# Kernel tuning notes

Measured on AMD Instinct MI355X. Metric: run time of the kernel, lower is better.

The kernel has to match this reference:

```python
import math
import jax, jax.numpy as jnp
import numpy as np

B, N, T, H = 4, 64, 384, 256
LAGS = (1, 5, 21)
L = len(LAGS)
NU = 500  # peer-universe size for rank buffers
TOPK = 8
LN_EPS = 1e-5


def setup_inputs() -> dict:
    key = jax.random.key(0)
    ks = jax.random.split(key, 24)
    s = 1.0 / np.sqrt(H)

    def lin(i):
        w = jax.random.uniform(ks[i], (H, H), jnp.float32, -s, s)
        b = jax.random.uniform(ks[i + 1], (H,), jnp.float32, -s, s)
        return w, b

    wq_w, wq_b = lin(0)
    wk_w, wk_b = lin(2)
    wv_w, wv_b = lin(4)
    f1_w, f1_b = lin(6)
    f2_w, f2_b = lin(8)
    return dict(
        target_h=jax.random.normal(ks[10], (B, T, H), jnp.float32),
        peer_h=jax.random.normal(ks[11], (B, N, T, H), jnp.float32),
        wq_w=wq_w, wq_b=wq_b, wk_w=wk_w, wk_b=wk_b, wv_w=wv_w, wv_b=wv_b,
        f1_w=f1_w, f1_b=f1_b, f2_w=f2_w, f2_b=f2_b,
        ln_g=jnp.ones((H,), jnp.float32),
        ln_b=jnp.zeros((H,), jnp.float32),
        alpha=jnp.float32(0.1),
        log_rank_strength=jnp.log(jnp.clip(jax.random.uniform(ks[12], (L, NU, NU)), 1e-6, None)),
        peer_mask=jnp.ones((B, N), dtype=bool),
        rank_topk_mask=jax.random.uniform(ks[13], (L, NU, NU)) < 0.2,
        target_id=jax.random.randint(ks[14], (B,), 0, NU),
        peer_id=jax.random.randint(ks[15], (B, N), 0, NU),
    )


def _forward(target_h, peer_h, wq_w, wq_b, wk_w, wk_b, wv_w, wv_b,
             f1_w, f1_b, f2_w, f2_b, ln_g, ln_b, alpha, log_rank_strength,
             peer_mask, rank_topk_mask, target_id, peer_id):
    lags = jnp.array(LAGS, dtype=jnp.int32)
    t_idx = jnp.arange(T, dtype=jnp.int32)[None, :] - lags[:, None]   # [L,T]
    valid_time = t_idx >= 0                                           # [L,T]
    t_idx_c = jnp.maximum(t_idx, 0)

    # lag-gathered peer features: [B,N,L,T,H] -> [B,T,N,L,H]
    peer_h_lag = jnp.transpose(peer_h[:, :, t_idx_c, :], (0, 3, 1, 2, 4))

    Q = target_h @ wq_w.T + wq_b                  # [B,T,H]
    K = peer_h_lag @ wk_w.T + wk_b                # [B,T,N,L,H]
    # delta-valued V path (use_delta_value=True): current minus lagged
    peer_h_now = jnp.transpose(peer_h, (0, 2, 1, 3))[:, :, :, None, :]  # [B,T,N,1,H]
    V = (peer_h_now - peer_h_lag) @ wv_w.T + wv_b  # [B,T,N,L,H]

    logits = jnp.einsum('bth,btnlh->btnl', Q, K) / math.sqrt(H)  # [B,T,N,L]

    # Bennett soft bias (use_bennett=True)
    tgt_b = jnp.broadcast_to(target_id[:, None], (B, N))          # [B,N]
    prior = jnp.transpose(log_rank_strength[:, peer_id, tgt_b], (1, 2, 0))  # [B,N,L]
    logits = logits + alpha * prior[:, None, :, :]

    neg_inf = jnp.float32(-jnp.inf)
    logits = jnp.where(valid_time.T[None, :, None, :], logits, neg_inf)      # time validity
    logits = jnp.where(peer_mask[:, None, :, None], logits, neg_inf)         # peer mask
    rmask = jnp.transpose(rank_topk_mask[:, peer_id, tgt_b], (1, 2, 0))      # [B,N,L]
    logits = jnp.where(rmask[:, None, :, :], logits, neg_inf)                # hard rank mask

    NL = N * L
    k = min(TOPK, NL)
    logits_flat = logits.reshape(B, T, NL)
    topk_vals, topk_idx = jax.lax.top_k(logits_flat, k)            # [B,T,k]
    is_inf = jnp.isinf(topk_vals)
    all_inf = jnp.all(is_inf, axis=-1, keepdims=True)
    topk_safe = jnp.where(is_inf, jnp.float32(-1e9), topk_vals)
    weights = jax.nn.softmax(topk_safe, axis=-1)
    weights = weights * (~all_inf).astype(weights.dtype)

    V_flat = V.reshape(B, T, NL, H)
    V_sel = jnp.take_along_axis(V_flat, topk_idx[..., None], axis=2)  # [B,T,k,H]
    ll_y = jnp.sum(weights[..., None] * V_sel, axis=2)                # [B,T,H]

    ffn = jax.nn.elu(ll_y @ f1_w.T + f1_b) @ f2_w.T + f2_b
    x = ll_y + ffn
    mu = jnp.mean(x, axis=-1, keepdims=True)
    var = jnp.var(x, axis=-1, keepdims=True)
    return (x - mu) / jnp.sqrt(var + LN_EPS) * ln_g + ln_b


def reference(target_h, peer_h, wq_w, wq_b, wk_w, wk_b, wv_w, wv_b,
              f1_w, f1_b, f2_w, f2_b, ln_g, ln_b, alpha, log_rank_strength,
              peer_mask, rank_topk_mask, target_id, peer_id):
    return _forward(target_h, peer_h, wq_w, wq_b, wk_w, wk_b, wv_w, wv_b,
                    f1_w, f1_b, f2_w, f2_b, ln_g, ln_b, alpha, log_rank_strength,
                    peer_mask, rank_topk_mask, target_id, peer_id)
```

## Files before the change

### kernel.cpp

```cpp
#include <hip/hip_runtime.h>
#include <hip/hip_bf16.h>


#define NU_ 500

__device__ __forceinline__ bool mask_at(const void* p, long i, int mode){
  if (mode == 1) return ((const unsigned char*)p)[i] != 0;
  if (mode == 2) return ((const unsigned short*)p)[i] != 0;
  return ((const unsigned int*)p)[i] != 0;
}

__global__ void prep_kernel(const float* __restrict__ lrs,
                            const void* __restrict__ pmask, const void* __restrict__ rmask,
                            const int* __restrict__ target_id, const int* __restrict__ peer_id,
                            const float* __restrict__ alpha_p,
                            float* __restrict__ prior)
{
  const int b = blockIdx.x;
  const int c = threadIdx.x;
  if (c >= 192) return;
  const unsigned char* pmB = (const unsigned char*)pmask;
  const unsigned char p0 = pmB[0], p1 = pmB[1];
  int mmode;
  if (p0 == 0x01u)      mmode = (p1 == 0x01u) ? 1 : 0;
  else if (p0 == 0x80u) mmode = 2;
  else                  mmode = 0;

  const int n = c / 3, l = c - n * 3;
  const int pid = peer_id[b * 64 + n];
  const int tgt = target_id[b];
  const long ridx = (long)l * (NU_*NU_) + (long)pid * NU_ + tgt;
  const bool ok = mask_at(pmask, b * 64 + n, mmode) && mask_at(rmask, ridx, mmode);
  prior[b * 192 + c] = ok ? alpha_p[0] * lrs[ridx] : -__builtin_inff();
}

__global__ __launch_bounds__(256) void qproj_kernel(
    const float* __restrict__ xg, const float* __restrict__ wq, const float* __restrict__ wqb,
    const float* __restrict__ wk, const float* __restrict__ wkb,
    float* __restrict__ Qt, float* __restrict__ qb)
{
  __shared__ __align__(16) float xs[8][256];
  __shared__ __align__(16) float qs[8][256];
  const int j = threadIdx.x;
  const int row0 = blockIdx.x * 8;
  #pragma unroll
  for (int r = 0; r < 8; ++r) xs[r][j] = xg[(long)(row0 + r) * 256 + j];
  __syncthreads();

  float acc[8];
  #pragma unroll
  for (int r = 0; r < 8; ++r) acc[r] = 0.f;
  const float4* wrow = (const float4*)(wq + (long)j * 256);
  for (int h8 = 0; h8 < 32; ++h8){
    float4 wa = wrow[h8 * 2], wb = wrow[h8 * 2 + 1];
    const int h = h8 * 8;
    #pragma unroll
    for (int r = 0; r < 8; ++r){
      const float* xr = &xs[r][h];
      acc[r] += xr[0]*wa.x + xr[1]*wa.y + xr[2]*wa.z + xr[3]*wa.w
              + xr[4]*wb.x + xr[5]*wb.y + xr[6]*wb.z + xr[7]*wb.w;
    }
  }
  const float bq = wqb[j];
  #pragma unroll
  for (int r = 0; r < 8; ++r) qs[r][j] = acc[r] + bq;
  __syncthreads();

  float at[8];
  #pragma unroll
  for (int r = 0; r < 8; ++r) at[r] = 0.f;
  for (int h = 0; h < 256; ++h){
    const float w = wk[(long)h * 256 + j];
    #pragma unroll
    for (int r = 0; r < 8; ++r) at[r] += qs[r][h] * w;
  }
  #pragma unroll
  for (int r = 0; r < 8; ++r) Qt[(long)(row0 + r) * 256 + j] = at[r];

  const float bk = wkb[j];
  #pragma unroll
  for (int r = 0; r < 8; ++r) xs[r][j] = qs[r][j] * bk;
  __syncthreads();
  if (j < 8){
    float s = 0.f;
    for (int h = 0; h < 256; ++h) s += xs[j][h];
    qb[row0 + j] = s;
  }
}

__global__ __launch_bounds__(256) void attn_kernel(
    const float* __restrict__ peer_h, const float* __restrict__ Qt,
    const float* __restrict__ qbv, const float* __restrict__ prior,
    float* __restrict__ dvec, float* __restrict__ ssum)
{
  __shared__ __align__(16) float qt_s[256];
  __shared__ float lg[192];
  __shared__ int   seli[8];
  __shared__ float selw[8];
  __shared__ int   allinf_sh;
  const int bt = blockIdx.x;
  const int b = bt / 384, t = bt % 384;
  const int tid = threadIdx.x;
  const float NEG_INF = -__builtin_inff();

  qt_s[tid] = Qt[(long)bt * 256 + tid];
  __syncthreads();
  const float qb = qbv[bt];
  const int lags[3] = {1, 5, 21};

  const int group = tid >> 4, q = tid & 15;
  float qv[16];
  #pragma unroll
  for (int i = 0; i < 4; ++i){
    float4 f = *(const float4*)&qt_s[q * 16 + i * 4];
    qv[i*4] = f.x; qv[i*4+1] = f.y; qv[i*4+2] = f.z; qv[i*4+3] = f.w;
  }

  #pragma unroll
  for (int it = 0; it < 12; ++it){
    const int c = it * 16 + group;
    const int n = c / 3, l = c - n * 3;
    const int lag = lags[l];
    const float pe = prior[b * 192 + c];
    const bool ok = (t >= lag) && (pe > -3.0e38f);
    float logit = NEG_INF;
    if (ok){
      const float4* rp = (const float4*)(peer_h + (((long)(b*64 + n)) * 384 + (t - lag)) * 256);
      float4 u0 = rp[q*4], u1 = rp[q*4+1], u2 = rp[q*4+2], u3 = rp[q*4+3];
      float p = u0.x*qv[0] + u0.y*qv[1] + u0.z*qv[2] + u0.w*qv[3]
              + u1.x*qv[4] + u1.y*qv[5] + u1.z*qv[6] + u1.w*qv[7]
              + u2.x*qv[8] + u2.y*qv[9] + u2.z*qv[10]+ u2.w*qv[11]
              + u3.x*qv[12]+ u3.y*qv[13]+ u3.z*qv[14]+ u3.w*qv[15];
      #pragma unroll
      for (int off = 1; off < 16; off <<= 1) p += __shfl_xor(p, off);
      logit = (p + qb) * 0.0625f + pe;
    }
    if (q == 0) lg[c] = logit;
  }
  __syncthreads();

  if (tid < 64){
    const int lane = tid;
    float v0 = lg[lane], v1 = lg[lane + 64], v2 = lg[lane + 128];
    float sv[8]; int si[8];
    for (int k = 0; k < 8; ++k){
      float mv = v0; int mi = lane;
      if (v1 > mv){ mv = v1; mi = lane + 64; }
      if (v2 > mv){ mv = v2; mi = lane + 128; }
      #pragma unroll
      for (int off = 32; off; off >>= 1){
        float ov = __shfl_xor(mv, off);
        int   oi = __shfl_xor(mi, off);
        if (ov > mv || (ov == mv && oi < mi)){ mv = ov; mi = oi; }
      }
      sv[k] = mv; si[k] = mi;
      if      (mi == lane)       v0 = NEG_INF;
      else if (mi == lane + 64)  v1 = NEG_INF;
      else if (mi == lane + 128) v2 = NEG_INF;
    }
    const int allinf = (sv[0] == NEG_INF) ? 1 : 0;
    const float m = allinf ? -1e9f : sv[0];
    float e[8]; float tot = 0.f;
    #pragma unroll
    for (int k = 0; k < 8; ++k){
      const float s = (sv[k] == NEG_INF) ? -1e9f : sv[k];
      e[k] = expf(s - m);
      tot += e[k];
    }
    if (lane == 0){
      allinf_sh = allinf;
      const float inv = 1.f / tot;
      for (int k = 0; k < 8; ++k){
        seli[k] = si[k];
        selw[k] = allinf ? 0.f : e[k] * inv;
      }
    }
  }
  __syncthreads();

  float acc = 0.f;
  const int h = tid;
  #pragma unroll
  for (int k = 0; k < 8; ++k){
    const float w = selw[k];
    if (w != 0.f){
      const int c = seli[k];
      const int n = c / 3, l = c - n * 3;
      const int tc = t - lags[l];
      const long base = ((long)(b*64 + n)) * 384;
      acc += w * (peer_h[(base + t ) * 256 + h]
                - peer_h[(base + tc) * 256 + h]);
    }
  }
  dvec[(long)bt * 256 + h] = acc;
  if (tid == 0) ssum[bt] = allinf_sh ? 0.f : 1.f;
}

__global__ __launch_bounds__(256) void ffn_kernel(
    const float* __restrict__ dv, const float* __restrict__ sv,
    const float* __restrict__ wv, const float* __restrict__ wvb,
    const float* __restrict__ f1, const float* __restrict__ f1b,
    const float* __restrict__ f2, const float* __restrict__ f2b,
    const float* __restrict__ lng, const float* __restrict__ lnb,
    float* __restrict__ out)
{
  __shared__ __align__(16) float ds[8][256];
  __shared__ __align__(16) float ys[8][256];
  __shared__ float mu_s[8], rs_s[8];
  const int j = threadIdx.x;
  const int row0 = blockIdx.x * 8;
  #pragma unroll
  for (int r = 0; r < 8; ++r) ds[r][j] = dv[(long)(row0 + r) * 256 + j];
  __syncthreads();

  float ll[8];
  {
    #pragma unroll
    for (int r = 0; r < 8; ++r) ll[r] = 0.f;
    const float4* wrow = (const float4*)(wv + (long)j * 256);
    for (int h8 = 0; h8 < 32; ++h8){
      float4 wa = wrow[h8 * 2], wb = wrow[h8 * 2 + 1];
      const int h = h8 * 8;
      #pragma unroll
      for (int r = 0; r < 8; ++r){
        const float* xr = &ds[r][h];
        ll[r] += xr[0]*wa.x + xr[1]*wa.y + xr[2]*wa.z + xr[3]*wa.w
               + xr[4]*wb.x + xr[5]*wb.y + xr[6]*wb.z + xr[7]*wb.w;
      }
    }
    const float bv = wvb[j];
    #pragma unroll
    for (int r = 0; r < 8; ++r) ll[r] += sv[row0 + r] * bv;
  }
  #pragma unroll
  for (int r = 0; r < 8; ++r) ys[r][j] = ll[r];
  __syncthreads();

  {
    float a[8];
    #pragma unroll
    for (int r = 0; r < 8; ++r) a[r] = 0.f;
    const float4* wrow = (const float4*)(f1 + (long)j * 256);
    for (int h8 = 0; h8 < 32; ++h8){
      float4 wa = wrow[h8 * 2], wb = wrow[h8 * 2 + 1];
      const int h = h8 * 8;
      #pragma unroll
      for (int r = 0; r < 8; ++r){
        const float* xr = &ys[r][h];
        a[r] += xr[0]*wa.x + xr[1]*wa.y + xr[2]*wa.z + xr[3]*wa.w
              + xr[4]*wb.x + xr[5]*wb.y + xr[6]*wb.z + xr[7]*wb.w;
      }
    }
    const float b1 = f1b[j];
    #pragma unroll
    for (int r = 0; r < 8; ++r){
      const float x = a[r] + b1;
      ds[r][j] = (x > 0.f) ? x : expm1f(x);
    }
  }
  __syncthreads();

  float xv[8];
  {
    float a[8];
    #pragma unroll
    for (int r = 0; r < 8; ++r) a[r] = 0.f;
    const float4* wrow = (const float4*)(f2 + (long)j * 256);
    for (int h8 = 0; h8 < 32; ++h8){
      float4 wa = wrow[h8 * 2], wb = wrow[h8 * 2 + 1];
      const int h = h8 * 8;
      #pragma unroll
      for (int r = 0; r < 8; ++r){
        const float* xr = &ds[r][h];
        a[r] += xr[0]*wa.x + xr[1]*wa.y + xr[2]*wa.z + xr[3]*wa.w
              + xr[4]*wb.x + xr[5]*wb.y + xr[6]*wb.z + xr[7]*wb.w;
      }
    }
    const float b2_ = f2b[j];
    #pragma unroll
    for (int r = 0; r < 8; ++r) xv[r] = ll[r] + a[r] + b2_;
  }
  #pragma unroll
  for (int r = 0; r < 8; ++r) ys[r][j] = xv[r];
  __syncthreads();

  {
    const int lane = j & 63, wvi = j >> 6;
    for (int rr = 0; rr < 2; ++rr){
      const int r = wvi * 2 + rr;
      float s = 0.f, qq = 0.f;
      for (int p = lane; p < 256; p += 64){ const float x = ys[r][p]; s += x; qq += x * x; }
      #pragma unroll
      for (int off = 32; off; off >>= 1){ s += __shfl_xor(s, off); qq += __shfl_xor(qq, off); }
      if (lane == 0){
        const float mu = s * (1.f/256.f);
        const float var = qq * (1.f/256.f) - mu * mu;
        mu_s[r] = mu; rs_s[r] = rsqrtf(var + 1e-5f);
      }
    }
  }
  __syncthreads();
  const float gj = lng[j], bj = lnb[j];
  #pragma unroll
  for (int r = 0; r < 8; ++r){
    const float o = (ys[r][j] - mu_s[r]) * rs_s[r] * gj + bj;
    out[(long)(row0 + r) * 256 + j] = o;
  }
}

extern "C" void kernel_launch(void* const* d_in, const int* in_sizes, int n_in,
                              void* d_out, int out_size, void* d_ws, size_t ws_size,
                              hipStream_t stream)
{
  (void)in_sizes; (void)n_in; (void)out_size; (void)ws_size;
  const float* target_h = (const float*)d_in[0];
  const float* peer_h   = (const float*)d_in[1];
  const float* wq_w = (const float*)d_in[2];  const float* wq_b = (const float*)d_in[3];
  const float* wk_w = (const float*)d_in[4];  const float* wk_b = (const float*)d_in[5];
  const float* wv_w = (const float*)d_in[6];  const float* wv_b = (const float*)d_in[7];
  const float* f1_w = (const float*)d_in[8];  const float* f1_b = (const float*)d_in[9];
  const float* f2_w = (const float*)d_in[10]; const float* f2_b = (const float*)d_in[11];
  const float* ln_g = (const float*)d_in[12]; const float* ln_b = (const float*)d_in[13];
  const float* alpha = (const float*)d_in[14];
  const float* lrs  = (const float*)d_in[15];
  const void* pmask = d_in[16];
  const void* rmask = d_in[17];
  const int* target_id = (const int*)d_in[18];
  const int* peer_id   = (const int*)d_in[19];

  float* prior = (float*)d_ws;
  float* Qt    = prior + 4 * 192;
  float* qb    = Qt + 393216;
  float* dvec  = qb + 1536;
  float* ssum  = dvec + 393216;

  prep_kernel<<<4, 192, 0, stream>>>(lrs, pmask, rmask, target_id, peer_id, alpha, prior);
  qproj_kernel<<<192, 256, 0, stream>>>(target_h, wq_w, wq_b, wk_w, wk_b, Qt, qb);
  attn_kernel<<<1536, 256, 0, stream>>>(peer_h, Qt, qb, prior, dvec, ssum);
  ffn_kernel<<<192, 256, 0, stream>>>(dvec, ssum, wv_w, wv_b, f1_w, f1_b,
                                      f2_w, f2_b, ln_g, ln_b, (float*)d_out);
}
```

Measured before the change: 269.6 us.

## Compact valid peer-lag candidates via ballot and merge prep into qproj kernel

The prior-computation kernel is folded into the Q-projection launch as four extra blocks, which removes one kernel launch. In the attention kernel, the candidates that pass the lag and prior checks are compacted into a dense index list with wave ballots, so the 16-thread groups loop only over valid candidates instead of a fixed 12 iterations with branches. The gather of selected V entries becomes branchless, using clamped indices. This adds two barriers and extra shared memory, and with an all-true mask most candidates stay valid, so little work is skipped.

Measured after the change: 263.8 us (median of 2 runs). 2.1% less time.

```diff
diff --git a/kernel.cpp b/kernel.cpp
--- a/kernel.cpp
+++ b/kernel.cpp
@@ -9,36 +9,34 @@
   if (mode == 2) return ((const unsigned short*)p)[i] != 0;
   return ((const unsigned int*)p)[i] != 0;
 }
-
-__global__ void prep_kernel(const float* __restrict__ lrs,
-                            const void* __restrict__ pmask, const void* __restrict__ rmask,
-                            const int* __restrict__ target_id, const int* __restrict__ peer_id,
-                            const float* __restrict__ alpha_p,
-                            float* __restrict__ prior)
-{
-  const int b = blockIdx.x;
-  const int c = threadIdx.x;
-  if (c >= 192) return;
-  const unsigned char* pmB = (const unsigned char*)pmask;
-  const unsigned char p0 = pmB[0], p1 = pmB[1];
-  int mmode;
-  if (p0 == 0x01u)      mmode = (p1 == 0x01u) ? 1 : 0;
-  else if (p0 == 0x80u) mmode = 2;
-  else                  mmode = 0;
-
-  const int n = c / 3, l = c - n * 3;
-  const int pid = peer_id[b * 64 + n];
-  const int tgt = target_id[b];
-  const long ridx = (long)l * (NU_*NU_) + (long)pid * NU_ + tgt;
-  const bool ok = mask_at(pmask, b * 64 + n, mmode) && mask_at(rmask, ridx, mmode);
-  prior[b * 192 + c] = ok ? alpha_p[0] * lrs[ridx] : -__builtin_inff();
-}
-
-__global__ __launch_bounds__(256) void qproj_kernel(
+__device__ __forceinline__ int lag_of(int l){ return (l == 0) ? 1 : ((l == 1) ? 5 : 21); }
+
+__global__ __launch_bounds__(256) void qproj_prep_kernel(
     const float* __restrict__ xg, const float* __restrict__ wq, const float* __restrict__ wqb,
     const float* __restrict__ wk, const float* __restrict__ wkb,
-    float* __restrict__ Qt, float* __restrict__ qb)
+    const float* __restrict__ lrs, const void* __restrict__ pmask, const void* __restrict__ rmask,
+    const int* __restrict__ target_id, const int* __restrict__ peer_id,
+    const float* __restrict__ alpha_p,
+    float* __restrict__ Qt, float* __restrict__ qb, float* __restrict__ prior)
 {
+  if (blockIdx.x >= 192){
+    const int b = blockIdx.x - 192;
+    const int c = threadIdx.x;
+    if (c >= 192) return;
+    const unsigned char* pmB = (const unsigned char*)pmask;
+    const unsigned char p0 = pmB[0], p1 = pmB[1];
+    int mmode;
+    if (p0 == 0x01u)      mmode = (p1 == 0x01u) ? 1 : 0;
+    else if (p0 == 0x80u) mmode = 2;
+    else                  mmode = 0;
+    const int n = c / 3, l = c - n * 3;
+    const int pid = peer_id[b * 64 + n];
+    const int tgt = target_id[b];
+    const long ridx = (long)l * (NU_*NU_) + (long)pid * NU_ + tgt;
+    const bool ok = mask_at(pmask, b * 64 + n, mmode) && mask_at(rmask, ridx, mmode);
+    prior[b * 192 + c] = ok ? alpha_p[0] * lrs[ridx] : -__builtin_inff();
+    return;
+  }
   __shared__ __align__(16) float xs[8][256];
   __shared__ __align__(16) float qs[8][256];
   const int j = threadIdx.x;
@@ -94,20 +92,41 @@
     float* __restrict__ dvec, float* __restrict__ ssum)
 {
   __shared__ __align__(16) float qt_s[256];
+  __shared__ float pr_s[192];
   __shared__ float lg[192];
+  __shared__ int   ix_s[192];
+  __shared__ int   wcnt[4];
   __shared__ int   seli[8];
   __shared__ float selw[8];
   __shared__ int   allinf_sh;
   const int bt = blockIdx.x;
   const int b = bt / 384, t = bt % 384;
   const int tid = threadIdx.x;
+  const int lane = tid & 63, wvi = tid >> 6;
   const float NEG_INF = -__builtin_inff();
 
   qt_s[tid] = Qt[(long)bt * 256 + tid];
-  __syncthreads();
+  bool valid = false;
+  if (tid < 192){
+    pr_s[tid] = prior[b * 192 + tid];
+    lg[tid] = NEG_INF;
+    ix_s[tid] = 1000 + tid;
+    const int l = tid - (tid / 3) * 3;
+    valid = (t >= lag_of(l)) && (pr_s[tid] > -3.0e38f);
+  }
+  const unsigned long long bal = __ballot(valid);
+  if (lane == 0) wcnt[wvi] = __popcll(bal);
+  __syncthreads();
+  const int cnt = wcnt[0] + wcnt[1] + wcnt[2];
+  if (valid){
+    int base = 0;
+    for (int i = 0; i < wvi; ++i) base += wcnt[i];
+    const int pos = base + __popcll(bal & ((1ULL << lane) - 1ULL));
+    ix_s[pos] = tid;
+  }
+  __syncthreads();
+
   const float qb = qbv[bt];
-  const int lags[3] = {1, 5, 21};
-
   const int group = tid >> 4, q = tid & 15;
   float qv[16];
   #pragma unroll
@@ -116,47 +135,41 @@
     qv[i*4] = f.x; qv[i*4+1] = f.y; qv[i*4+2] = f.z; qv[i*4+3] = f.w;
   }
 
-  #pragma unroll
-  for (int it = 0; it < 12; ++it){
-    const int c = it * 16 + group;
+  for (int i = group; i < cnt; i += 16){
+    const int c = ix_s[i];
     const int n = c / 3, l = c - n * 3;
-    const int lag = lags[l];
-    const float pe = prior[b * 192 + c];
-    const bool ok = (t >= lag) && (pe > -3.0e38f);
-    float logit = NEG_INF;
-    if (ok){
-      const float4* rp = (const float4*)(peer_h + (((long)(b*64 + n)) * 384 + (t - lag)) * 256);
-      float4 u0 = rp[q*4], u1 = rp[q*4+1], u2 = rp[q*4+2], u3 = rp[q*4+3];
-      float p = u0.x*qv[0] + u0.y*qv[1] + u0.z*qv[2] + u0.w*qv[3]
-              + u1.x*qv[4] + u1.y*qv[5] + u1.z*qv[6] + u1.w*qv[7]
-              + u2.x*qv[8] + u2.y*qv[9] + u2.z*qv[10]+ u2.w*qv[11]
-              + u3.x*qv[12]+ u3.y*qv[13]+ u3.z*qv[14]+ u3.w*qv[15];
-      #pragma unroll
-      for (int off = 1; off < 16; off <<= 1) p += __shfl_xor(p, off);
-      logit = (p + qb) * 0.0625f + pe;
-    }
-    if (q == 0) lg[c] = logit;
+    const int tc = t - lag_of(l);
+    const float4* rp = (const float4*)(peer_h + (((long)(b*64 + n)) * 384 + tc) * 256);
+    float4 u0 = rp[q*4], u1 = rp[q*4+1], u2 = rp[q*4+2], u3 = rp[q*4+3];
+    float p = u0.x*qv[0] + u0.y*qv[1] + u0.z*qv[2] + u0.w*qv[3]
+            + u1.x*qv[4] + u1.y*qv[5] + u1.z*qv[6] + u1.w*qv[7]
+            + u2.x*qv[8] + u2.y*qv[9] + u2.z*qv[10]+ u2.w*qv[11]
+            + u3.x*qv[12]+ u3.y*qv[13]+ u3.z*qv[14]+ u3.w*qv[15];
+    #pragma unroll
+    for (int off = 1; off < 16; off <<= 1) p += __shfl_xor(p, off);
+    if (q == 0) lg[i] = (p + qb) * 0.0625f + pr_s[c];
   }
   __syncthreads();
 
   if (tid < 64){
-    const int lane = tid;
     float v0 = lg[lane], v1 = lg[lane + 64], v2 = lg[lane + 128];
+    int   i0 = ix_s[lane], i1 = ix_s[lane + 64], i2 = ix_s[lane + 128];
     float sv[8]; int si[8];
     for (int k = 0; k < 8; ++k){
-      float mv = v0; int mi = lane;
-      if (v1 > mv){ mv = v1; mi = lane + 64; }
-      if (v2 > mv){ mv = v2; mi = lane + 128; }
+      float mv = v0; int mi = i0; int ms = 0;
+      if (v1 > mv || (v1 == mv && i1 < mi)){ mv = v1; mi = i1; ms = 1; }
+      if (v2 > mv || (v2 == mv && i2 < mi)){ mv = v2; mi = i2; ms = 2; }
       #pragma unroll
       for (int off = 32; off; off >>= 1){
         float ov = __shfl_xor(mv, off);
         int   oi = __shfl_xor(mi, off);
-        if (ov > mv || (ov == mv && oi < mi)){ mv = ov; mi = oi; }
+        int   os = __shfl_xor(ms, off);
+        if (ov > mv || (ov == mv && oi < mi)){ mv = ov; mi = oi; ms = os; }
       }
       sv[k] = mv; si[k] = mi;
-      if      (mi == lane)       v0 = NEG_INF;
-      else if (mi == lane + 64)  v1 = NEG_INF;
-      else if (mi == lane + 128) v2 = NEG_INF;
+      if (mi == i0 && ms == 0)      v0 = NEG_INF;
+      else if (mi == i1 && ms == 1) v1 = NEG_INF;
+      else if (mi == i2 && ms == 2) v2 = NEG_INF;
     }
     const int allinf = (sv[0] == NEG_INF) ? 1 : 0;
     const float m = allinf ? -1e9f : sv[0];
@@ -183,14 +196,12 @@
   #pragma unroll
   for (int k = 0; k < 8; ++k){
     const float w = selw[k];
-    if (w != 0.f){
-      const int c = seli[k];
-      const int n = c / 3, l = c - n * 3;
-      const int tc = t - lags[l];
-      const long base = ((long)(b*64 + n)) * 384;
-      acc += w * (peer_h[(base + t ) * 256 + h]
-                - peer_h[(base + tc) * 256 + h]);
-    }
+    const int c = min(seli[k], 191);
+    const int n = c / 3, l = c - n * 3;
+    const int tc = max(t - lag_of(l), 0);
+    const long base = ((long)(b*64 + n)) * 384;
+    acc += w * (peer_h[(base + t ) * 256 + h]
+              - peer_h[(base + tc) * 256 + h]);
   }
   dvec[(long)bt * 256 + h] = acc;
   if (tid == 0) ssum[bt] = allinf_sh ? 0.f : 1.f;
@@ -334,8 +345,8 @@
   float* dvec  = qb + 1536;
   float* ssum  = dvec + 393216;
 
-  prep_kernel<<<4, 192, 0, stream>>>(lrs, pmask, rmask, target_id, peer_id, alpha, prior);
-  qproj_kernel<<<192, 256, 0, stream>>>(target_h, wq_w, wq_b, wk_w, wk_b, Qt, qb);
+  qproj_prep_kernel<<<196, 256, 0, stream>>>(target_h, wq_w, wq_b, wk_w, wk_b,
+      lrs, pmask, rmask, target_id, peer_id, alpha, Qt, qb, prior);
   attn_kernel<<<1536, 256, 0, stream>>>(peer_h, Qt, qb, prior, dvec, ssum);
   ffn_kernel<<<192, 256, 0, stream>>>(dvec, ssum, wv_w, wv_b, f1_w, f1_b,
                                       f2_w, f2_b, ln_g, ln_b, (float*)d_out);
```
